# Performance work log

Measured on AMD Instinct MI355X. Metric: run time of the kernel, lower is better.

Reference implementation:

```python
import jax, jax.numpy as jnp
import numpy as np

B, S, D = 2, 2048, 4096
H, KVH, DH = 32, 8, 128
KVD = KVH * DH  # 1024
EPS = 1e-6
SCALING = DH ** -0.5


def _rms_norm(x, scale):
    xf = x.astype(jnp.float32)
    var = jnp.mean(xf * xf, axis=-1, keepdims=True)
    return (xf * jax.lax.rsqrt(var + EPS)).astype(x.dtype) * scale


def _rotate_half(x):
    half = x.shape[-1] // 2
    return jnp.concatenate([-x[..., half:], x[..., :half]], axis=-1)


def setup_inputs() -> dict:
    key = jax.random.key(0)
    ks = jax.random.split(key, 5)
    hidden_states = jax.random.normal(ks[0], (B, S, D), dtype=jnp.float32)
    w_qkv = jax.random.normal(ks[1], (D, D + 2 * KVD), dtype=jnp.float32) * 0.02
    w_out = jax.random.normal(ks[2], (D, D), dtype=jnp.float32) * 0.02
    q_scale = jnp.ones((D,), dtype=jnp.float32)
    k_scale = jnp.ones((KVD,), dtype=jnp.float32)
    # real rotary tables: cos/sin of positions, broadcast to batch
    inv_freq = 1.0 / (10000.0 ** (np.arange(0, DH, 2, dtype=np.float32) / DH))
    pos = np.arange(S, dtype=np.float32)
    freqs = np.outer(pos, inv_freq)            # [S, DH/2]
    emb = np.concatenate([freqs, freqs], -1)   # [S, DH]
    cos_cached = jnp.broadcast_to(jnp.asarray(np.cos(emb)), (B, S, DH))
    sin_cached = jnp.broadcast_to(jnp.asarray(np.sin(emb)), (B, S, DH))
    # causal mask: True = masked
    idx = jnp.arange(S)
    attention_mask = (idx[None, :] > idx[:, None])[None, None].repeat(B, 0)  # [B,1,S,S] bool
    return {
        "hidden_states": hidden_states, "w_qkv": w_qkv, "w_out": w_out,
        "q_scale": q_scale, "k_scale": k_scale,
        "cos_cached": cos_cached, "sin_cached": sin_cached,
        "attention_mask": attention_mask,
    }


def reference(hidden_states, w_qkv, w_out, q_scale, k_scale, cos_cached, sin_cached, attention_mask):
    b, s, _ = hidden_states.shape
    qkv = jnp.einsum("bsd,de->bse", hidden_states, w_qkv)
    q, k, v = jnp.split(qkv, [D, D + KVD], axis=-1)
    # qk-norm applied pre-view over full projected dim (non-qwen3 path)
    q = _rms_norm(q, q_scale)
    k = _rms_norm(k, k_scale)
    q = q.reshape(b, s, H, DH).transpose(0, 2, 1, 3)    # [B,H,S,DH]
    k = k.reshape(b, s, KVH, DH).transpose(0, 2, 1, 3)  # [B,KVH,S,DH]
    v = v.reshape(b, s, KVH, DH).transpose(0, 2, 1, 3)
    cos = cos_cached[:, None]  # [B,1,S,DH]
    sin = sin_cached[:, None]
    q = q * cos + _rotate_half(q) * sin
    k = k * cos + _rotate_half(k) * sin
    # repeat KV heads to match query heads (GQA)
    n_rep = H // KVH
    k = jnp.repeat(k, n_rep, axis=1)
    v = jnp.repeat(v, n_rep, axis=1)
    scores = jnp.einsum("bhsd,bhtd->bhst", q, k) * SCALING
    scores = jnp.where(attention_mask, jnp.float32(-10000.0), scores)
    attn = jax.nn.softmax(scores.astype(jnp.float32), axis=-1).astype(q.dtype)
    out = jnp.einsum("bhst,bhtd->bhsd", attn, v)
    out = out.transpose(0, 2, 1, 3).reshape(b, s, H * DH)
    return jnp.einsum("bsd,de->bse", out, w_out)
```

## Files before the change

### kernel.cpp

```cpp
#include <hip/hip_runtime.h>
#include <hip/hip_bf16.h>
#include <cstdint>
#include <cstddef>

#define BB 2
#define SS 2048
#define DD 4096
#define HH 32
#define KVH 8
#define DH 128
#define KVD 1024
#define SCALE 0.08838834764831845f
#define QSC 0.1275178745225f

typedef __attribute__((ext_vector_type(8))) short short8;
typedef __attribute__((ext_vector_type(4))) float f32x4;

typedef __attribute__((address_space(1))) void GV;
typedef __attribute__((address_space(3))) void LV;

__device__ __forceinline__ void async16(const void* g, void* l) {
  __builtin_amdgcn_global_load_lds((GV*)g, (LV*)l, 16, 0, 0);
}

__device__ __forceinline__ unsigned short f2bf(float x) {
  union { float f; uint32_t u; } v; v.f = x;
  uint32_t r = (v.u + 0x7fffu + ((v.u >> 16) & 1u)) >> 16;
  return (unsigned short)r;
}
__device__ __forceinline__ float bf2f(unsigned short b) {
  union { uint32_t u; float f; } v; v.u = ((uint32_t)b) << 16; return v.f;
}
__device__ __forceinline__ f32x4 mfma16(short8 a, short8 b, f32x4 c) {
  return __builtin_amdgcn_mfma_f32_16x16x32_bf16(a, b, c, 0, 0, 0);
}

__global__ __launch_bounds__(256) void cast_bf16_kernel(
    const float* __restrict__ in, unsigned short* __restrict__ out, int n4) {
  int i = blockIdx.x * 256 + threadIdx.x;
  if (i >= n4) return;
  float4 v = ((const float4*)in)[i];
  ushort4 o;
  o.x = f2bf(v.x); o.y = f2bf(v.y); o.z = f2bf(v.z); o.w = f2bf(v.w);
  ((ushort4*)out)[i] = o;
}

__global__ __launch_bounds__(256) void transpose_cast_kernel(
    const float* __restrict__ in, unsigned short* __restrict__ out, int R, int C) {
  __shared__ unsigned short tile[32][33];
  const int tx = threadIdx.x, ty = threadIdx.y;
  const int c0 = blockIdx.x * 32, r0 = blockIdx.y * 32;
  for (int i = ty; i < 32; i += 8)
    tile[i][tx] = f2bf(in[(size_t)(r0 + i) * C + c0 + tx]);
  __syncthreads();
  for (int i = ty; i < 32; i += 8)
    out[(size_t)(c0 + i) * R + r0 + tx] = tile[tx][i];
}

__global__ __launch_bounds__(256) void transpose_v_kernel(
    const unsigned short* __restrict__ qkv, unsigned short* __restrict__ vo) {
  __shared__ unsigned short tile[32][33];
  const int s0 = blockIdx.x * 32, d0 = blockIdx.y * 32;
  const int b = blockIdx.z >> 3, kvh = blockIdx.z & 7;
  const int tx = threadIdx.x, ty = threadIdx.y;
  const unsigned short* ip = qkv + 5120 + (size_t)kvh * 128 + d0 + tx;
  for (int i = ty; i < 32; i += 8)
    tile[i][tx] = ip[(size_t)(b * SS + s0 + i) * 6144];
  __syncthreads();
  unsigned short* op = vo + (size_t)(b * KVH + kvh) * DH * SS + s0 + tx;
  for (int i = ty; i < 32; i += 8)
    op[(size_t)(d0 + i) * SS] = tile[tx][i];
}

template <typename OutT>
__global__ __launch_bounds__(256, 2) void gemm_bt(
    const unsigned short* __restrict__ A, const unsigned short* __restrict__ Bt,
    OutT* __restrict__ C, int M, int N, int K) {
  __shared__ __align__(16) unsigned short As[4096];
  __shared__ __align__(16) unsigned short Bs[4096];
  const int tid = threadIdx.x;
  const int wave = tid >> 6, lane = tid & 63, quad = lane >> 4, l16 = lane & 15;
  const int m0 = blockIdx.x * 128, n0 = blockIdx.y * 128;
  const int wm = (wave & 1) * 64, wn = (wave >> 1) * 64;
  f32x4 acc[4][4] = {};
  const int sr = tid >> 2;
  const int sg = (tid & 3) ^ ((tid >> 3) & 3);
  const unsigned short* Ag = A + (size_t)(m0 + sr) * K + sg * 8;
  const unsigned short* Bg = Bt + (size_t)(n0 + sr) * K + sg * 8;
  unsigned short* AsW = As + wave * 512;
  unsigned short* BsW = Bs + wave * 512;
  const int pg = (quad ^ ((l16 >> 1) & 3)) * 8;
  for (int k0 = 0; k0 < K; k0 += 32) {
    __syncthreads();
    async16(Ag + k0, AsW);
    async16(Ag + (size_t)64 * K + k0, AsW + 2048);
    async16(Bg + k0, BsW);
    async16(Bg + (size_t)64 * K + k0, BsW + 2048);
    __syncthreads();
    short8 af[4], bf[4];
#pragma unroll
    for (int i = 0; i < 4; i++) {
      af[i] = *(const short8*)&As[(wm + i * 16 + l16) * 32 + pg];
      bf[i] = *(const short8*)&Bs[(wn + i * 16 + l16) * 32 + pg];
    }
#pragma unroll
    for (int mi = 0; mi < 4; mi++)
#pragma unroll
      for (int ni = 0; ni < 4; ni++)
        acc[mi][ni] = mfma16(af[mi], bf[ni], acc[mi][ni]);
  }
#pragma unroll
  for (int mi = 0; mi < 4; mi++)
#pragma unroll
    for (int ni = 0; ni < 4; ni++)
#pragma unroll
      for (int r = 0; r < 4; r++) {
        int row = m0 + wm + mi * 16 + quad * 4 + r;
        int col = n0 + wn + ni * 16 + l16;
        float v = acc[mi][ni][r];
        if constexpr (sizeof(OutT) == 4) C[(size_t)row * N + col] = v;
        else                             C[(size_t)row * N + col] = (OutT)f2bf(v);
      }
}

__global__ __launch_bounds__(256) void rmsnorm_rope_kernel(
    const unsigned short* __restrict__ qkv,
    const float* __restrict__ q_scale, const float* __restrict__ k_scale,
    const float* __restrict__ cosc, const float* __restrict__ sinc,
    unsigned short* __restrict__ qo,
    unsigned short* __restrict__ ko)
{
  const int row = blockIdx.x;
  const int b = row >> 11, s = row & 2047;
  const int tid = threadIdx.x;
  const unsigned short* qr = qkv + (size_t)row * 6144;
  short8 qv0 = *(const short8*)&qr[tid * 8];
  short8 qv1 = *(const short8*)&qr[2048 + tid * 8];
  ushort4 kv = *(const ushort4*)&qr[4096 + tid * 4];
  float sq = 0.f, sk = 0.f;
#pragma unroll
  for (int e = 0; e < 8; e++) {
    float a = bf2f((unsigned short)qv0[e]); sq += a * a;
    float c = bf2f((unsigned short)qv1[e]); sq += c * c;
  }
  float kf[4];
#pragma unroll
  for (int e = 0; e < 4; e++) {
    kf[e] = bf2f(((const unsigned short*)&kv)[e]); sk += kf[e] * kf[e];
  }
#pragma unroll
  for (int off = 32; off; off >>= 1) {
    sq += __shfl_down(sq, off, 64);
    sk += __shfl_down(sk, off, 64);
  }
  __shared__ float redq[4], redk[4];
  if ((tid & 63) == 0) { redq[tid >> 6] = sq; redk[tid >> 6] = sk; }
  __syncthreads();
  sq = redq[0] + redq[1] + redq[2] + redq[3];
  sk = redk[0] + redk[1] + redk[2] + redk[3];
  const float rq = rsqrtf(sq * (1.f / 4096.f) + 1e-6f);
  const float rk = rsqrtf(sk * (1.f / 1024.f) + 1e-6f);
  const float* cp = cosc + (size_t)row * 128;
  const float* sp = sinc + (size_t)row * 128;
#pragma unroll
  for (int it = 0; it < 2; it++) {
    const int c = it * 2048 + tid * 8;
    const int d = c & 127, hh = c >> 7;
    short8 v8 = it ? qv1 : qv0;
    short8 p8 = *(const short8*)&qr[c ^ 64];
    const float sgn = (d < 64) ? -1.f : 1.f;
    ushort o8[8];
#pragma unroll
    for (int e = 0; e < 8; e++) {
      float v = bf2f((unsigned short)v8[e]) * rq * q_scale[c + e];
      float p = bf2f((unsigned short)p8[e]) * rq * q_scale[(c ^ 64) + e];
      o8[e] = f2bf((v * cp[d + e] + sgn * p * sp[d + e]) * QSC);
    }
    *(uint4*)&qo[((size_t)(b * HH + hh) * SS + s) * DH + d] = *(const uint4*)o8;
  }
  {
    const int c = tid * 4;
    const int d = c & 127, hh = c >> 7;
    ushort4 p4 = *(const ushort4*)&qr[4096 + (c ^ 64)];
    const float sgn = (d < 64) ? -1.f : 1.f;
    ushort o4[4];
#pragma unroll
    for (int e = 0; e < 4; e++) {
      float v = kf[e] * rk * k_scale[c + e];
      float p = bf2f(((const unsigned short*)&p4)[e]) * rk * k_scale[(c ^ 64) + e];
      o4[e] = f2bf(v * cp[d + e] + sgn * p * sp[d + e]);
    }
    *(uint2*)&ko[((size_t)(b * KVH + hh) * SS + s) * DH + d] = *(const uint2*)o4;
  }
}

__global__ __launch_bounds__(256, 2) void flash_attn(
    const unsigned short* __restrict__ Q,
    const unsigned short* __restrict__ Kr,
    const unsigned short* __restrict__ Vt,
    unsigned short* __restrict__ O)
{
  __shared__ __align__(16) unsigned short Ks[8192];
  __shared__ __align__(16) unsigned short Vs[8192];
  __shared__ __align__(16) unsigned int   Ps[4][1024];
  const int tid = threadIdx.x, wave = tid >> 6, lane = tid & 63;
  const int quad = lane >> 4, l16 = lane & 15;
  const int bh = blockIdx.x, b = bh >> 5, h = bh & 31;
  const int kvh = h >> 2;
  const int qbase = ((int)gridDim.y - 1 - (int)blockIdx.y) * 128;
  const unsigned short* Qb = Q + (size_t)(b * HH + h) * SS * DH;
  short8 qf[2][4];
#pragma unroll
  for (int mi = 0; mi < 2; mi++) {
    const unsigned short* Qp = Qb + (size_t)(qbase + mi * 64 + wave * 16 + l16) * DH + quad * 8;
#pragma unroll
    for (int c = 0; c < 4; c++) qf[mi][c] = *(const short8*)(Qp + c * 32);
  }
  const unsigned short* Kg = Kr + (size_t)(b * KVH + kvh) * SS * DH;
  const unsigned short* Vg = Vt + (size_t)(b * KVH + kvh) * DH * SS;
  int bK[4], bV[4];
#pragma unroll
  for (int j = 0; j < 4; j++) {
    const int kk = wave * 16 + j * 4 + quad;
    const int gd = l16 ^ ((j * 4 + quad) & 15);
    bK[j] = kk * 128 + gd * 8;
    const int dd = (wave * 4 + j) * 8 + (lane >> 3);
    const int gk = (lane & 7) ^ ((lane >> 3) & 7);
    bV[j] = dd * 2048 + gk * 8;
  }
  f32x4 o[2][8] = {};
  float m_i[2] = {-1e30f, -1e30f}, l_i[2] = {0.f, 0.f};
  const int ndiag = qbase >> 6;
  const int nkt = ndiag + 2;
  for (int kt = 0; kt < nkt; kt++) {
    const int k0 = kt * 64;
    __syncthreads();
#pragma unroll
    for (int j = 0; j < 4; j++) {
      async16(Kg + (size_t)k0 * 128 + bK[j], Ks + (wave * 4 + j) * 512);
      async16(Vg + k0 + bV[j], Vs + (wave * 4 + j) * 512);
    }
    __syncthreads();
    f32x4 st[4][2] = {};
#pragma unroll
    for (int km = 0; km < 4; km++) {
      const unsigned short* krow = Ks + (km * 16 + l16) * 128;
#pragma unroll
      for (int c = 0; c < 4; c++) {
        short8 kf = *(const short8*)(krow + (((c * 4 + quad) ^ l16) * 8));
        st[km][0] = mfma16(kf, qf[0][c], st[km][0]);
        st[km][1] = mfma16(kf, qf[1][c], st[km][1]);
      }
    }
    const bool mtile = (kt >= ndiag);
    float alpha[2];
#pragma unroll
    for (int mi = 0; mi < 2; mi++) {
      if (mtile) {
        const int qg = qbase + mi * 64 + wave * 16 + l16;
#pragma unroll
        for (int km = 0; km < 4; km++)
#pragma unroll
          for (int r = 0; r < 4; r++)
            if (k0 + km * 16 + quad * 4 + r > qg) st[km][mi][r] = -1e4f;
      }
      float tmax = -3e38f;
#pragma unroll
      for (int km = 0; km < 4; km++)
#pragma unroll
        for (int r = 0; r < 4; r++) tmax = fmaxf(tmax, st[km][mi][r]);
      tmax = fmaxf(tmax, __shfl_xor(tmax, 16, 64));
      tmax = fmaxf(tmax, __shfl_xor(tmax, 32, 64));
      const float mn = fmaxf(m_i[mi], tmax);
      alpha[mi] = __builtin_amdgcn_exp2f(m_i[mi] - mn);
      m_i[mi] = mn;
      float rs = 0.f;
#pragma unroll
      for (int km = 0; km < 4; km++)
#pragma unroll
        for (int r = 0; r < 4; r++) {
          float e = __builtin_amdgcn_exp2f(st[km][mi][r] - mn);
          st[km][mi][r] = e;
          rs += e;
        }
      rs += __shfl_xor(rs, 16, 64);
      rs += __shfl_xor(rs, 32, 64);
      l_i[mi] = l_i[mi] * alpha[mi] + rs;
      unsigned int* pw = &Ps[wave][(mi * 16 + l16) * 32 + (quad & 1) * 2];
#pragma unroll
      for (int km = 0; km < 4; km++) {
        const int g = (km * 2 + (quad >> 1)) ^ (l16 & 7);
        float e0 = st[km][mi][0], e1 = st[km][mi][1], e2 = st[km][mi][2], e3 = st[km][mi][3];
        pw[g * 4]     = __builtin_amdgcn_perm(__builtin_bit_cast(unsigned int, e1),
                                              __builtin_bit_cast(unsigned int, e0), 0x07060302u);
        pw[g * 4 + 1] = __builtin_amdgcn_perm(__builtin_bit_cast(unsigned int, e3),
                                              __builtin_bit_cast(unsigned int, e2), 0x07060302u);
      }
    }
    if (__any((alpha[0] != 1.f) || (alpha[1] != 1.f))) {
#pragma unroll
      for (int mi = 0; mi < 2; mi++) {
        float ar[4];
#pragma unroll
        for (int r = 0; r < 4; r++)
          ar[r] = __shfl(alpha[mi], (lane & 48) + quad * 4 + r, 64);
#pragma unroll
        for (int f = 0; f < 8; f++)
#pragma unroll
          for (int r = 0; r < 4; r++) o[mi][f][r] *= ar[r];
      }
    }
#pragma unroll
    for (int kc = 0; kc < 2; kc++) {
      short8 pa[2];
#pragma unroll
      for (int mi = 0; mi < 2; mi++) {
        const int g = (kc * 4 + quad) ^ (l16 & 7);
        uint4 pv4 = *(const uint4*)&Ps[wave][(mi * 16 + l16) * 32 + g * 4];
        pa[mi] = __builtin_bit_cast(short8, pv4);
      }
#pragma unroll
      for (int f = 0; f < 8; f++) {
        const int d = f * 16 + l16;
        short8 vf = *(const short8*)(Vs + d * 64 + (((kc * 4 + quad) ^ (l16 & 7)) * 8));
        o[0][f] = mfma16(pa[0], vf, o[0][f]);
        o[1][f] = mfma16(pa[1], vf, o[1][f]);
      }
    }
  }
  float il[2][4];
#pragma unroll
  for (int mi = 0; mi < 2; mi++)
#pragma unroll
    for (int r = 0; r < 4; r++) {
      float lv = __shfl(l_i[mi], (lane & 48) + quad * 4 + r, 64);
      il[mi][r] = 1.f / lv;
    }
#pragma unroll
  for (int mi = 0; mi < 2; mi++) {
    unsigned short* Op = O + (size_t)(b * SS + qbase + mi * 64 + wave * 16 + quad * 4) * DD + h * DH + l16;
#pragma unroll
    for (int f = 0; f < 8; f++)
#pragma unroll
      for (int r = 0; r < 4; r++)
        Op[(size_t)r * DD + f * 16] = f2bf(o[mi][f][r] * il[mi][r]);
  }
}

extern "C" void kernel_launch(void* const* d_in, const int* in_sizes, int n_in,
                              void* d_out, int out_size, void* d_ws, size_t ws_size,
                              hipStream_t stream) {
  const float* hs      = (const float*)d_in[0];
  const float* wqkv    = (const float*)d_in[1];
  const float* wout    = (const float*)d_in[2];
  const float* q_scale = (const float*)d_in[3];
  const float* k_scale = (const float*)d_in[4];
  const float* cosc    = (const float*)d_in[5];
  const float* sinc    = (const float*)d_in[6];
  float* out = (float*)d_out;

  unsigned short* ws = (unsigned short*)d_ws;
  unsigned short* wqkvT = ws;
  unsigned short* woutT = wqkvT + 25165824;
  unsigned short* hsb   = woutT + 16777216;
  unsigned short* qkv   = hsb + 16777216;
  unsigned short* qrope = wqkvT;
  unsigned short* krope = wqkvT + 16777216;
  unsigned short* vT    = wqkvT + 16777216 + 4194304;
  unsigned short* attno = hsb;

  cast_bf16_kernel<<<16384, 256, 0, stream>>>(hs, hsb, 4194304);
  transpose_cast_kernel<<<dim3(192, 128), dim3(32, 8), 0, stream>>>(wqkv, wqkvT, 4096, 6144);
  transpose_cast_kernel<<<dim3(128, 128), dim3(32, 8), 0, stream>>>(wout, woutT, 4096, 4096);
  gemm_bt<unsigned short><<<dim3(32, 48), 256, 0, stream>>>(hsb, wqkvT, qkv, 4096, 6144, 4096);
  rmsnorm_rope_kernel<<<4096, 256, 0, stream>>>(qkv, q_scale, k_scale, cosc, sinc,
                                                qrope, krope);
  transpose_v_kernel<<<dim3(64, 4, 16), dim3(32, 8), 0, stream>>>(qkv, vT);
  flash_attn<<<dim3(64, 16), 256, 0, stream>>>(qrope, krope, vT, attno);
  gemm_bt<float><<<dim3(32, 32), 256, 0, stream>>>(attno, woutT, out, 4096, 4096, 4096);
}
```

Measured before the change: 799.6 us.

## Double-buffer K/V tiles in flash attention and transpose PV MFMA output

```diff
diff --git a/kernel.cpp b/kernel.cpp
--- a/kernel.cpp
+++ b/kernel.cpp
@@ -200,8 +200,8 @@
     const unsigned short* __restrict__ Vt,
     unsigned short* __restrict__ O)
 {
-  __shared__ __align__(16) unsigned short Ks[8192];
-  __shared__ __align__(16) unsigned short Vs[8192];
+  __shared__ __align__(16) unsigned short Ks[2][8192];
+  __shared__ __align__(16) unsigned short Vs[2][8192];
   __shared__ __align__(16) unsigned int   Ps[4][1024];
   const int tid = threadIdx.x, wave = tid >> 6, lane = tid & 63;
   const int quad = lane >> 4, l16 = lane & 15;
@@ -232,19 +232,28 @@
   float m_i[2] = {-1e30f, -1e30f}, l_i[2] = {0.f, 0.f};
   const int ndiag = qbase >> 6;
   const int nkt = ndiag + 2;
+  unsigned short *Kc = &Ks[0][0], *Kn = &Ks[1][0];
+  unsigned short *Vc = &Vs[0][0], *Vn = &Vs[1][0];
+#pragma unroll
+  for (int j = 0; j < 4; j++) {
+    async16(Kg + bK[j], Kc + (wave * 4 + j) * 512);
+    async16(Vg + bV[j], Vc + (wave * 4 + j) * 512);
+  }
   for (int kt = 0; kt < nkt; kt++) {
     const int k0 = kt * 64;
-    __syncthreads();
-#pragma unroll
-    for (int j = 0; j < 4; j++) {
-      async16(Kg + (size_t)k0 * 128 + bK[j], Ks + (wave * 4 + j) * 512);
-      async16(Vg + k0 + bV[j], Vs + (wave * 4 + j) * 512);
-    }
-    __syncthreads();
+    asm volatile("s_waitcnt vmcnt(0)\n\ts_barrier" ::: "memory");
+    if (kt + 1 < nkt) {
+      const int k1 = k0 + 64;
+#pragma unroll
+      for (int j = 0; j < 4; j++) {
+        async16(Kg + (size_t)k1 * 128 + bK[j], Kn + (wave * 4 + j) * 512);
+        async16(Vg + k1 + bV[j], Vn + (wave * 4 + j) * 512);
+      }
+    }
     f32x4 st[4][2] = {};
 #pragma unroll
     for (int km = 0; km < 4; km++) {
-      const unsigned short* krow = Ks + (km * 16 + l16) * 128;
+      const unsigned short* krow = Kc + (km * 16 + l16) * 128;
 #pragma unroll
       for (int c = 0; c < 4; c++) {
         short8 kf = *(const short8*)(krow + (((c * 4 + quad) ^ l16) * 8));
@@ -299,17 +308,13 @@
     }
     if (__any((alpha[0] != 1.f) || (alpha[1] != 1.f))) {
 #pragma unroll
-      for (int mi = 0; mi < 2; mi++) {
-        float ar[4];
-#pragma unroll
-        for (int r = 0; r < 4; r++)
-          ar[r] = __shfl(alpha[mi], (lane & 48) + quad * 4 + r, 64);
+      for (int mi = 0; mi < 2; mi++)
 #pragma unroll
         for (int f = 0; f < 8; f++)
 #pragma unroll
-          for (int r = 0; r < 4; r++) o[mi][f][r] *= ar[r];
-      }
-    }
+          for (int r = 0; r < 4; r++) o[mi][f][r] *= alpha[mi];
+    }
+    asm volatile("s_waitcnt lgkmcnt(0)" ::: "memory");
 #pragma unroll
     for (int kc = 0; kc < 2; kc++) {
       short8 pa[2];
@@ -322,28 +327,29 @@
 #pragma unroll
       for (int f = 0; f < 8; f++) {
         const int d = f * 16 + l16;
-        short8 vf = *(const short8*)(Vs + d * 64 + (((kc * 4 + quad) ^ (l16 & 7)) * 8));
-        o[0][f] = mfma16(pa[0], vf, o[0][f]);
-        o[1][f] = mfma16(pa[1], vf, o[1][f]);
-      }
-    }
-  }
-  float il[2][4];
-#pragma unroll
-  for (int mi = 0; mi < 2; mi++)
-#pragma unroll
-    for (int r = 0; r < 4; r++) {
-      float lv = __shfl(l_i[mi], (lane & 48) + quad * 4 + r, 64);
-      il[mi][r] = 1.f / lv;
-    }
+        short8 vf = *(const short8*)(Vc + d * 64 + (((kc * 4 + quad) ^ (l16 & 7)) * 8));
+        o[0][f] = mfma16(vf, pa[0], o[0][f]);
+        o[1][f] = mfma16(vf, pa[1], o[1][f]);
+      }
+    }
+    unsigned short* t;
+    t = Kc; Kc = Kn; Kn = t;
+    t = Vc; Vc = Vn; Vn = t;
+  }
 #pragma unroll
   for (int mi = 0; mi < 2; mi++) {
-    unsigned short* Op = O + (size_t)(b * SS + qbase + mi * 64 + wave * 16 + quad * 4) * DD + h * DH + l16;
-#pragma unroll
-    for (int f = 0; f < 8; f++)
-#pragma unroll
-      for (int r = 0; r < 4; r++)
-        Op[(size_t)r * DD + f * 16] = f2bf(o[mi][f][r] * il[mi][r]);
+    const float il = 1.f / l_i[mi];
+    unsigned short* Op = O + (size_t)(b * SS + qbase + mi * 64 + wave * 16 + l16) * DD
+                       + h * DH + quad * 4;
+#pragma unroll
+    for (int f = 0; f < 8; f++) {
+      unsigned int lo = (unsigned int)f2bf(o[mi][f][0] * il)
+                      | ((unsigned int)f2bf(o[mi][f][1] * il) << 16);
+      unsigned int hi = (unsigned int)f2bf(o[mi][f][2] * il)
+                      | ((unsigned int)f2bf(o[mi][f][3] * il) << 16);
+      uint2 pk; pk.x = lo; pk.y = hi;
+      *(uint2*)(Op + f * 16) = pk;
+    }
   }
 }
 
```

Measured after the change: 815.6 us. 1.02x slower.
